# Performance work log

Measured on AMD Instinct MI355X. Metric: run time of the kernel, lower is better.

## Reference

```python
import jax, jax.numpy as jnp
import numpy as np

E = 1024
H = 16
D = E // H
MLP = 4096
EPS = 1e-5


def _layernorm(x, g, b):
    mu = jnp.mean(x, axis=-1, keepdims=True)
    var = jnp.mean(jnp.square(x - mu), axis=-1, keepdims=True)
    return (x - mu) * jax.lax.rsqrt(var + EPS) * g + b


def setup_inputs() -> dict:
    key = jax.random.key(0)
    ks = jax.random.split(key, 10)
    s = lambda fan_in: 1.0 / np.sqrt(fan_in)
    return {
        "x": jax.random.normal(ks[0], (4, 2048, E), dtype=jnp.float32),
        "qkv_w": jax.random.uniform(ks[1], (3 * E, E), jnp.float32, -s(E), s(E)),
        "fc_w": jax.random.uniform(ks[2], (E, E), jnp.float32, -s(E), s(E)),
        "fc_b": jax.random.uniform(ks[3], (E,), jnp.float32, -s(E), s(E)),
        "ln1_g": jnp.ones((E,), jnp.float32),
        "ln1_b": jnp.zeros((E,), jnp.float32),
        "ln2_g": jnp.ones((E,), jnp.float32),
        "ln2_b": jnp.zeros((E,), jnp.float32),
        "w1": jax.random.uniform(ks[4], (MLP, E), jnp.float32, -s(E), s(E)),
        "b1": jax.random.uniform(ks[5], (MLP,), jnp.float32, -s(E), s(E)),
        "w2": jax.random.uniform(ks[6], (E, MLP), jnp.float32, -s(MLP), s(MLP)),
        "b2": jax.random.uniform(ks[7], (E,), jnp.float32, -s(MLP), s(MLP)),
    }


def reference(x, qkv_w, fc_w, fc_b, ln1_g, ln1_b, ln2_g, ln2_b, w1, b1, w2, b2):
    B, S, _ = x.shape
    scale = D ** (-0.5)
    # --- attention sublayer ---
    h = _layernorm(x, ln1_g, ln1_b)
    qkv = (h @ qkv_w.T).reshape(B, S, 3, H, D)
    q, k, v = jnp.moveaxis(qkv, 2, 0)            # each [B, S, H, D]
    q = q.transpose(0, 2, 1, 3)                  # [B, H, S, D]
    k = k.transpose(0, 2, 1, 3)
    v = v.transpose(0, 2, 1, 3)
    scores = jnp.einsum("bhqd,bhkd->bhqk", q, k) * scale
    attn = jax.nn.softmax(scores, axis=-1)
    out = jnp.einsum("bhqk,bhkd->bhqd", attn, v)
    out = out.transpose(0, 2, 1, 3).reshape(B, S, E)
    x = x + (out @ fc_w.T + fc_b)
    # --- MLP sublayer ---
    h = _layernorm(x, ln2_g, ln2_b)
    h = jax.nn.gelu(h @ w1.T + b1, approximate=False)
    x = x + (h @ w2.T + b2)
    return x
```

## Files before the change

### kernel.cpp

```cpp
#include <hip/hip_runtime.h>
#include <cstdint>
#include <cmath>

#define EDIM 1024
#define SEQ 2048
#define BATCH 4
#define NHEAD 16
#define HDIM 64
#define MLPD 4096
#define ROWS 8192

typedef unsigned short u16;
typedef __attribute__((ext_vector_type(8))) short short8;
typedef __attribute__((ext_vector_type(4))) float floatx4;

#define AS1 __attribute__((address_space(1)))
#define AS3 __attribute__((address_space(3)))

#define Q_SCALE 0.18033688011112042f

__device__ __forceinline__ void async16(const void* g, void* l) {
  __builtin_amdgcn_global_load_lds((AS1 void*)g, (AS3 void*)l, 16, 0, 0);
}

__device__ __forceinline__ u16 f2bf(float f) {
  union { float f; unsigned int u; } v; v.f = f;
  unsigned int u = v.u;
  u += 0x7fffu + ((u >> 16) & 1u);
  return (u16)(u >> 16);
}

__device__ __forceinline__ unsigned int u32of(float f) {
  union { float f; unsigned int u; } v; v.f = f; return v.u;
}

__device__ __forceinline__ unsigned int pack_trunc(float a, float b) {
  return __builtin_amdgcn_perm(u32of(b), u32of(a), 0x07060302u);
}

__device__ __forceinline__ float exp2_fast(float x) {
  return __builtin_amdgcn_exp2f(x);
}

__device__ __forceinline__ float gelu_f(float x) {
  const float y = 0.7978845608028654f * (x + 0.044715f * x * x * x);
  const float e = exp2_fast(y * 2.885390081777927f);
  const float t = 1.0f - 2.0f * __builtin_amdgcn_rcpf(1.0f + e);
  return 0.5f * x * (1.0f + t);
}

__global__ __launch_bounds__(256) void cvt_bf16(const float* __restrict__ in,
                                                u16* __restrict__ outp, int n) {
  const int i = (blockIdx.x * 256 + threadIdx.x) * 4;
  if (i >= n) return;
  const float4 v = *(const float4*)(in + i);
  outp[i + 0] = f2bf(v.x); outp[i + 1] = f2bf(v.y);
  outp[i + 2] = f2bf(v.z); outp[i + 3] = f2bf(v.w);
}

__global__ __launch_bounds__(256) void ln_bf16(const float* __restrict__ x,
                                               const float* __restrict__ g,
                                               const float* __restrict__ bta,
                                               u16* __restrict__ outp) {
  const int row = blockIdx.x;
  const int tid = threadIdx.x;
  const float4 v = *(const float4*)(x + (size_t)row * EDIM + tid * 4);
  float s = v.x + v.y + v.z + v.w;
  float ss = v.x * v.x + v.y * v.y + v.z * v.z + v.w * v.w;
#pragma unroll
  for (int o = 1; o < 64; o <<= 1) {
    s += __shfl_xor(s, o);
    ss += __shfl_xor(ss, o);
  }
  __shared__ float red[8];
  const int wave = tid >> 6, lane = tid & 63;
  if (lane == 0) { red[wave] = s; red[4 + wave] = ss; }
  __syncthreads();
  s = red[0] + red[1] + red[2] + red[3];
  ss = red[4] + red[5] + red[6] + red[7];
  const float mu = s * (1.0f / 1024.0f);
  const float var = ss * (1.0f / 1024.0f) - mu * mu;
  const float inv = rsqrtf(var + 1e-5f);
  const float4 gv = *(const float4*)(g + tid * 4);
  const float4 bv = *(const float4*)(bta + tid * 4);
  u16* od = outp + (size_t)row * EDIM + tid * 4;
  od[0] = f2bf((v.x - mu) * inv * gv.x + bv.x);
  od[1] = f2bf((v.y - mu) * inv * gv.y + bv.y);
  od[2] = f2bf((v.z - mu) * inv * gv.z + bv.z);
  od[3] = f2bf((v.w - mu) * inv * gv.w + bv.w);
}

template <int EPI>
__global__ __launch_bounds__(256) void gemm_bt(const u16* __restrict__ A,
                                               const u16* __restrict__ Bw,
                                               void* __restrict__ Cout,
                                               const float* __restrict__ bias,
                                               const float* __restrict__ res,
                                               int M, int N, int K) {
  __shared__ __align__(16) u16 As[128 * 64];
  __shared__ __align__(16) u16 Bs[128 * 64];
  const int tid = threadIdx.x;
  const int lane = tid & 63;
  const int wave = tid >> 6;
  const int quad = lane >> 4;
  const int cl = lane & 15;
  const int row0 = blockIdx.y * 128;
  const int col0 = blockIdx.x * 128;
  const int wm = wave >> 1;
  const int wn = wave & 1;

  floatx4 acc[4][4];
#pragma unroll
  for (int i = 0; i < 4; ++i)
#pragma unroll
    for (int j = 0; j < 4; ++j) acc[i][j] = (floatx4){0.f, 0.f, 0.f, 0.f};

  const int lrow = lane >> 3;
  const int gc = (lane & 7) ^ lrow;
  const u16* Ath = A + (size_t)(row0 + wave * 32 + lrow) * K + gc * 8;
  const u16* Bth = Bw + (size_t)(col0 + wave * 32 + lrow) * K + gc * 8;
  u16* lA = As + (wave * 256 + lane) * 8;
  u16* lB = Bs + (wave * 256 + lane) * 8;
  const size_t pstride = (size_t)8 * K;

  for (int k0 = 0; k0 < K; k0 += 64) {
    __syncthreads();
#pragma unroll
    for (int p = 0; p < 4; ++p) {
      async16(Ath + p * pstride + k0, lA + p * 512);
      async16(Bth + p * pstride + k0, lB + p * 512);
    }
    __syncthreads();
#pragma unroll
    for (int s = 0; s < 2; ++s) {
      short8 af[4], bfr[4];
      const int ko = ((s * 4 + quad) ^ (cl & 7)) * 8;
#pragma unroll
      for (int i = 0; i < 4; ++i)
        af[i] = *(const short8*)(As + (wm * 64 + i * 16 + cl) * 64 + ko);
#pragma unroll
      for (int j = 0; j < 4; ++j)
        bfr[j] = *(const short8*)(Bs + (wn * 64 + j * 16 + cl) * 64 + ko);
#pragma unroll
      for (int i = 0; i < 4; ++i)
#pragma unroll
        for (int j = 0; j < 4; ++j)
          acc[i][j] = __builtin_amdgcn_mfma_f32_16x16x32_bf16(af[i], bfr[j], acc[i][j], 0, 0, 0);
    }
  }

  const float qscale = (EPI == 5 && col0 < 1024) ? Q_SCALE : 1.0f;
#pragma unroll
  for (int i = 0; i < 4; ++i) {
#pragma unroll
    for (int r = 0; r < 4; ++r) {
      const int row = row0 + wm * 64 + i * 16 + quad * 4 + r;
#pragma unroll
      for (int j = 0; j < 4; ++j) {
        const int col = col0 + wn * 64 + j * 16 + cl;
        const size_t idx = (size_t)row * N + col;
        float v = acc[i][j][r];
        if (EPI == 0) {
          ((float*)Cout)[idx] = v;
        } else if (EPI == 1 || EPI == 3) {
          ((float*)Cout)[idx] = v + bias[col] + res[idx];
        } else if (EPI == 2) {
          ((u16*)Cout)[idx] = f2bf(gelu_f(v + bias[col]));
        } else if (EPI == 4) {
          ((u16*)Cout)[idx] = f2bf(v);
        } else if (EPI == 5) {
          ((u16*)Cout)[idx] = f2bf(v * qscale);
        }
      }
    }
  }
}

__global__ __launch_bounds__(256) void vtrans(const u16* __restrict__ qkv,
                                              u16* __restrict__ vt) {
  __shared__ unsigned int T[64 * 65];
  const int tid = threadIdx.x;
  const int bh = blockIdx.y;
  const int b = bh >> 4;
  const int h = bh & 15;
  const int s0 = blockIdx.x * 64;
#pragma unroll
  for (int pp = 0; pp < 2; ++pp) {
    const int g = pp * 256 + tid;
    const int r = g >> 3;
    const int d0 = (g & 7) * 8;
    const u16* src = qkv + (size_t)(b * SEQ + s0 + r) * 3072 + 2048 + h * 64 + d0;
    short8 v = *(const short8*)src;
#pragma unroll
    for (int i = 0; i < 8; ++i) T[(d0 + i) * 65 + r] = (u16)v[i];
  }
  __syncthreads();
#pragma unroll
  for (int pp = 0; pp < 2; ++pp) {
    const int g = pp * 256 + tid;
    const int d = g >> 3;
    const int sc = (g & 7) * 8;
    short8 v;
#pragma unroll
    for (int i = 0; i < 8; ++i) v[i] = (short)(u16)T[d * 65 + sc + i];
    *(short8*)(vt + ((size_t)bh * 64 + d) * SEQ + s0 + sc) = v;
  }
}

__global__ __launch_bounds__(256, 4) void attn3(const u16* __restrict__ qkv,
                                                const u16* __restrict__ vt,
                                                u16* __restrict__ outp) {
  __shared__ __align__(16) u16 smem[8192 + 8192 + 4 * 32 * 72];
  u16* Ks = smem;
  u16* Vs = smem + 8192;
  const int tid = threadIdx.x;
  const int lane = tid & 63;
  const int wave = tid >> 6;
  const int quad = lane >> 4;
  const int cl = lane & 15;

  const int f = blockIdx.y * 16 + blockIdx.x;
  const int xcd = f & 7;
  const int u = f >> 3;
  const int qi = u & 15;
  const int bh = xcd * 8 + (u >> 4);
  const int b = bh >> 4;
  const int h = bh & 15;
  const int q0 = qi * 128;
  u16* Pw = smem + 16384 + wave * (32 * 72);

  const u16* qbase = qkv + (size_t)(b * SEQ) * 3072 + h * 64;
  const u16* kbase = qbase + 1024;
  const u16* vbase = vt + (size_t)bh * 64 * SEQ;

#pragma unroll
  for (int p = 0; p < 4; ++p) {
    const int g = (wave * 4 + p) * 64 + lane;
    const int r = g >> 3;
    const int c = (g & 7) ^ (r & 7);
    async16(qbase + (size_t)(q0 + r) * 3072 + c * 8, smem + g * 8);
  }
  __syncthreads();
  short8 qf[2][2];
#pragma unroll
  for (int ng = 0; ng < 2; ++ng)
#pragma unroll
    for (int kc = 0; kc < 2; ++kc) {
      const int row = wave * 32 + ng * 16 + cl;
      qf[ng][kc] = *(const short8*)(smem + row * 64 + (((kc * 4 + quad) ^ (cl & 7)) * 8));
    }

  floatx4 O[4][2];
  float lrun[2] = {0.f, 0.f};
#pragma unroll
  for (int mg = 0; mg < 4; ++mg)
#pragma unroll
    for (int ng = 0; ng < 2; ++ng) O[mg][ng] = (floatx4){0.f, 0.f, 0.f, 0.f};

  for (int kt = 0; kt < SEQ / 128; ++kt) {
    const int k0 = kt * 128;
    __syncthreads();
    const u16* kb = kbase + (size_t)k0 * 3072;
#pragma unroll
    for (int p = 0; p < 2; ++p) {
      const int g = wave * 128 + p * 64 + lane;
      const int rk = g >> 3;
      const int ck = (g & 7) ^ (rk & 7);
      async16(kb + (size_t)rk * 3072 + ck * 8, Ks + g * 8);
      const int rv = g >> 4;
      const int cv = (g & 15) ^ (rv & 15);
      async16(vbase + (size_t)rv * SEQ + k0 + cv * 8, Vs + g * 8);
    }
    __syncthreads();

#pragma unroll
    for (int s = 0; s < 2; ++s) {
      floatx4 Sc[4][2];
#pragma unroll
      for (int mg = 0; mg < 4; ++mg)
#pragma unroll
        for (int ng = 0; ng < 2; ++ng) Sc[mg][ng] = (floatx4){0.f, 0.f, 0.f, 0.f};
#pragma unroll
      for (int kc = 0; kc < 2; ++kc) {
        short8 kf[4];
#pragma unroll
        for (int mg = 0; mg < 4; ++mg) {
          const int row = s * 64 + mg * 16 + cl;
          kf[mg] = *(const short8*)(Ks + row * 64 + (((kc * 4 + quad) ^ (cl & 7)) * 8));
        }
#pragma unroll
        for (int mg = 0; mg < 4; ++mg)
#pragma unroll
          for (int ng = 0; ng < 2; ++ng)
            Sc[mg][ng] = __builtin_amdgcn_mfma_f32_16x16x32_bf16(kf[mg], qf[ng][kc], Sc[mg][ng], 0, 0, 0);
      }

#pragma unroll
      for (int ng = 0; ng < 2; ++ng) {
        float rs = 0.f;
#pragma unroll
        for (int mg = 0; mg < 4; ++mg)
#pragma unroll
          for (int r = 0; r < 4; ++r) {
            const float pv = exp2_fast(Sc[mg][ng][r]);
            Sc[mg][ng][r] = pv;
            rs += pv;
          }
        rs += __shfl_xor(rs, 16);
        rs += __shfl_xor(rs, 32);
        lrun[ng] += rs;
      }

#pragma unroll
      for (int mg = 0; mg < 4; ++mg)
#pragma unroll
        for (int ng = 0; ng < 2; ++ng) {
          const unsigned int lo = pack_trunc(Sc[mg][ng][0], Sc[mg][ng][1]);
          const unsigned int hi = pack_trunc(Sc[mg][ng][2], Sc[mg][ng][3]);
          *(uint2*)(Pw + (ng * 16 + cl) * 72 + mg * 16 + quad * 4) = make_uint2(lo, hi);
        }

#pragma unroll
      for (int kc = 0; kc < 2; ++kc) {
        short8 pf[2], vf[4];
#pragma unroll
        for (int ng = 0; ng < 2; ++ng)
          pf[ng] = *(const short8*)(Pw + (ng * 16 + cl) * 72 + kc * 32 + quad * 8);
#pragma unroll
        for (int mg = 0; mg < 4; ++mg) {
          const int row = mg * 16 + cl;
          vf[mg] = *(const short8*)(Vs + row * 128 + (((s * 8 + kc * 4 + quad) ^ (cl & 15)) * 8));
        }
#pragma unroll
        for (int mg = 0; mg < 4; ++mg)
#pragma unroll
          for (int ng = 0; ng < 2; ++ng)
            O[mg][ng] = __builtin_amdgcn_mfma_f32_16x16x32_bf16(vf[mg], pf[ng], O[mg][ng], 0, 0, 0);
      }
    }
  }

#pragma unroll
  for (int ng = 0; ng < 2; ++ng) {
    const float inv = 1.0f / lrun[ng];
    const int qrow = q0 + wave * 32 + ng * 16 + cl;
    u16* od = outp + (size_t)(b * SEQ + qrow) * EDIM + h * 64;
#pragma unroll
    for (int mg = 0; mg < 4; ++mg) {
      const unsigned int lo = (unsigned int)f2bf(O[mg][ng][0] * inv) |
                              ((unsigned int)f2bf(O[mg][ng][1] * inv) << 16);
      const unsigned int hi = (unsigned int)f2bf(O[mg][ng][2] * inv) |
                              ((unsigned int)f2bf(O[mg][ng][3] * inv) << 16);
      *(uint2*)(od + mg * 16 + quad * 4) = make_uint2(lo, hi);
    }
  }
}

extern "C" void kernel_launch(void* const* d_in, const int* in_sizes, int n_in,
                              void* d_out, int out_size, void* d_ws, size_t ws_size,
                              hipStream_t stream) {
  const float* x    = (const float*)d_in[0];
  const float* qkvw = (const float*)d_in[1];
  const float* fcw  = (const float*)d_in[2];
  const float* fcb  = (const float*)d_in[3];
  const float* ln1g = (const float*)d_in[4];
  const float* ln1b = (const float*)d_in[5];
  const float* ln2g = (const float*)d_in[6];
  const float* ln2b = (const float*)d_in[7];
  const float* w1   = (const float*)d_in[8];
  const float* b1   = (const float*)d_in[9];
  const float* w2   = (const float*)d_in[10];
  const float* b2   = (const float*)d_in[11];

  char* ws = (char*)d_ws;
  size_t off = 0;
  u16* wqkv = (u16*)(ws + off); off += (size_t)3 * EDIM * EDIM * 2;
  u16* wfc  = (u16*)(ws + off); off += (size_t)EDIM * EDIM * 2;
  u16* w1b  = (u16*)(ws + off); off += (size_t)MLPD * EDIM * 2;
  u16* w2b  = (u16*)(ws + off); off += (size_t)EDIM * MLPD * 2;
  u16* hbuf = (u16*)(ws + off); off += (size_t)ROWS * EDIM * 2;
  u16* aout = (u16*)(ws + off); off += (size_t)ROWS * EDIM * 2;
  float* x2 = (float*)(ws + off); off += (size_t)ROWS * EDIM * 4;
  u16* qkvb = (u16*)(ws + off); off += (size_t)ROWS * 3 * EDIM * 2;
  u16* vtb  = (u16*)(ws + off); off += (size_t)ROWS * EDIM * 2;
  u16* hmlp = qkvb;

  cvt_bf16<<<3072, 256, 0, stream>>>(qkvw, wqkv, 3 * EDIM * EDIM);
  cvt_bf16<<<1024, 256, 0, stream>>>(fcw, wfc, EDIM * EDIM);
  cvt_bf16<<<4096, 256, 0, stream>>>(w1, w1b, MLPD * EDIM);
  cvt_bf16<<<4096, 256, 0, stream>>>(w2, w2b, EDIM * MLPD);

  ln_bf16<<<ROWS, 256, 0, stream>>>(x, ln1g, ln1b, hbuf);
  gemm_bt<5><<<dim3(24, 64), 256, 0, stream>>>(hbuf, wqkv, qkvb, nullptr, nullptr,
                                               ROWS, 3 * EDIM, EDIM);
  vtrans<<<dim3(SEQ / 64, 64), 256, 0, stream>>>(qkvb, vtb);
  attn3<<<dim3(16, 64), 256, 0, stream>>>(qkvb, vtb, aout);
  gemm_bt<1><<<dim3(8, 64), 256, 0, stream>>>(aout, wfc, x2, fcb, x,
                                              ROWS, EDIM, EDIM);
  ln_bf16<<<ROWS, 256, 0, stream>>>(x2, ln2g, ln2b, hbuf);
  gemm_bt<2><<<dim3(32, 64), 256, 0, stream>>>(hbuf, w1b, hmlp, b1, nullptr,
                                               ROWS, MLPD, EDIM);
  gemm_bt<3><<<dim3(8, 64), 256, 0, stream>>>(hmlp, w2b, (float*)d_out, b2, x2,
                                              ROWS, EDIM, MLPD);
}
```

Before: 556.5 us.

## Enlarge GEMM tiles to 256x128 with 512 threads and merge weight conversions

The bf16 GEMM now uses 8 waves per block and covers 256 rows instead of 128. Each weight tile loaded into LDS is reused across twice as many rows, and the global-to-LDS load indexing is reworked to match. The four fp32-to-bf16 weight conversion launches become a single kernel that picks its source by index range, cutting launch overhead. The trade-off is that the N=1024 GEMMs drop to 256 blocks, which risks poor CU fill and load balance, and each block uses more LDS.

```diff
diff --git a/kernel.cpp b/kernel.cpp
--- a/kernel.cpp
+++ b/kernel.cpp
@@ -49,13 +49,20 @@
   return 0.5f * x * (1.0f + t);
 }
 
-__global__ __launch_bounds__(256) void cvt_bf16(const float* __restrict__ in,
-                                                u16* __restrict__ outp, int n) {
-  const int i = (blockIdx.x * 256 + threadIdx.x) * 4;
-  if (i >= n) return;
-  const float4 v = *(const float4*)(in + i);
-  outp[i + 0] = f2bf(v.x); outp[i + 1] = f2bf(v.y);
-  outp[i + 2] = f2bf(v.z); outp[i + 3] = f2bf(v.w);
+__global__ __launch_bounds__(256) void cvt_all(const float* __restrict__ a, u16* __restrict__ oa, int na,
+                                               const float* __restrict__ b, u16* __restrict__ ob, int nb,
+                                               const float* __restrict__ c, u16* __restrict__ oc, int nc,
+                                               const float* __restrict__ d, u16* __restrict__ od) {
+  int i = (blockIdx.x * 256 + threadIdx.x) * 4;
+  const float* src;
+  u16* dst;
+  if (i < na) { src = a; dst = oa; }
+  else if ((i -= na) < nb) { src = b; dst = ob; }
+  else if ((i -= nb) < nc) { src = c; dst = oc; }
+  else { i -= nc; src = d; dst = od; }
+  const float4 v = *(const float4*)(src + i);
+  dst[i + 0] = f2bf(v.x); dst[i + 1] = f2bf(v.y);
+  dst[i + 2] = f2bf(v.z); dst[i + 3] = f2bf(v.w);
 }
 
 __global__ __launch_bounds__(256) void ln_bf16(const float* __restrict__ x,
@@ -91,20 +98,20 @@
 }
 
 template <int EPI>
-__global__ __launch_bounds__(256) void gemm_bt(const u16* __restrict__ A,
+__global__ __launch_bounds__(512) void gemm_bt(const u16* __restrict__ A,
                                                const u16* __restrict__ Bw,
                                                void* __restrict__ Cout,
                                                const float* __restrict__ bias,
                                                const float* __restrict__ res,
                                                int M, int N, int K) {
-  __shared__ __align__(16) u16 As[128 * 64];
+  __shared__ __align__(16) u16 As[256 * 64];
   __shared__ __align__(16) u16 Bs[128 * 64];
   const int tid = threadIdx.x;
   const int lane = tid & 63;
   const int wave = tid >> 6;
   const int quad = lane >> 4;
   const int cl = lane & 15;
-  const int row0 = blockIdx.y * 128;
+  const int row0 = blockIdx.y * 256;
   const int col0 = blockIdx.x * 128;
   const int wm = wave >> 1;
   const int wn = wave & 1;
@@ -115,26 +122,27 @@
 #pragma unroll
     for (int j = 0; j < 4; ++j) acc[i][j] = (floatx4){0.f, 0.f, 0.f, 0.f};
 
-  const int lrow = lane >> 3;
-  const int gc = (lane & 7) ^ lrow;
-  const u16* Ath = A + (size_t)(row0 + wave * 32 + lrow) * K + gc * 8;
-  const u16* Bth = Bw + (size_t)(col0 + wave * 32 + lrow) * K + gc * 8;
-  u16* lA = As + (wave * 256 + lane) * 8;
-  u16* lB = Bs + (wave * 256 + lane) * 8;
-  const size_t pstride = (size_t)8 * K;
+  const int trow = tid >> 3;
+  const int gc = (tid & 7) ^ (trow & 7);
+  const u16* Ath = A + (size_t)(row0 + trow) * K + gc * 8;
+  const u16* Bth = Bw + (size_t)(col0 + trow) * K + gc * 8;
+  u16* lA = As + tid * 8;
+  u16* lB = Bs + tid * 8;
+  const size_t pstride = (size_t)64 * K;
 
   for (int k0 = 0; k0 < K; k0 += 64) {
     __syncthreads();
 #pragma unroll
-    for (int p = 0; p < 4; ++p) {
-      async16(Ath + p * pstride + k0, lA + p * 512);
-      async16(Bth + p * pstride + k0, lB + p * 512);
-    }
+    for (int p = 0; p < 4; ++p)
+      async16(Ath + p * pstride + k0, lA + p * 4096);
+#pragma unroll
+    for (int p = 0; p < 2; ++p)
+      async16(Bth + p * pstride + k0, lB + p * 4096);
     __syncthreads();
 #pragma unroll
     for (int s = 0; s < 2; ++s) {
+      const int ko = ((s * 4 + quad) ^ (cl & 7)) * 8;
       short8 af[4], bfr[4];
-      const int ko = ((s * 4 + quad) ^ (cl & 7)) * 8;
 #pragma unroll
       for (int i = 0; i < 4; ++i)
         af[i] = *(const short8*)(As + (wm * 64 + i * 16 + cl) * 64 + ko);
@@ -385,21 +393,21 @@
   u16* vtb  = (u16*)(ws + off); off += (size_t)ROWS * EDIM * 2;
   u16* hmlp = qkvb;
 
-  cvt_bf16<<<3072, 256, 0, stream>>>(qkvw, wqkv, 3 * EDIM * EDIM);
-  cvt_bf16<<<1024, 256, 0, stream>>>(fcw, wfc, EDIM * EDIM);
-  cvt_bf16<<<4096, 256, 0, stream>>>(w1, w1b, MLPD * EDIM);
-  cvt_bf16<<<4096, 256, 0, stream>>>(w2, w2b, EDIM * MLPD);
+  cvt_all<<<12288, 256, 0, stream>>>(qkvw, wqkv, 3 * EDIM * EDIM,
+                                     fcw, wfc, EDIM * EDIM,
+                                     w1, w1b, MLPD * EDIM,
+                                     w2, w2b);
 
   ln_bf16<<<ROWS, 256, 0, stream>>>(x, ln1g, ln1b, hbuf);
-  gemm_bt<5><<<dim3(24, 64), 256, 0, stream>>>(hbuf, wqkv, qkvb, nullptr, nullptr,
+  gemm_bt<5><<<dim3(24, 32), 512, 0, stream>>>(hbuf, wqkv, qkvb, nullptr, nullptr,
                                                ROWS, 3 * EDIM, EDIM);
   vtrans<<<dim3(SEQ / 64, 64), 256, 0, stream>>>(qkvb, vtb);
   attn3<<<dim3(16, 64), 256, 0, stream>>>(qkvb, vtb, aout);
-  gemm_bt<1><<<dim3(8, 64), 256, 0, stream>>>(aout, wfc, x2, fcb, x,
+  gemm_bt<1><<<dim3(8, 32), 512, 0, stream>>>(aout, wfc, x2, fcb, x,
                                               ROWS, EDIM, EDIM);
   ln_bf16<<<ROWS, 256, 0, stream>>>(x2, ln2g, ln2b, hbuf);
-  gemm_bt<2><<<dim3(32, 64), 256, 0, stream>>>(hbuf, w1b, hmlp, b1, nullptr,
+  gemm_bt<2><<<dim3(32, 32), 512, 0, stream>>>(hbuf, w1b, hmlp, b1, nullptr,
                                                ROWS, MLPD, EDIM);
-  gemm_bt<3><<<dim3(8, 64), 256, 0, stream>>>(hmlp, w2b, (float*)d_out, b2, x2,
+  gemm_bt<3><<<dim3(8, 32), 512, 0, stream>>>(hmlp, w2b, (float*)d_out, b2, x2,
                                               ROWS, EDIM, MLPD);
 }
```

Result: faster. 522.5 us (-6.1%).
